# Optimization experiments

Hardware: AMD Instinct MI355X
Metric: run time of the kernel (lower is better)

## Reference

```python
import jax, jax.numpy as jnp
import numpy as np

B, S_IMG, S_TXT, P, D, HEADS, HD = 1, 2048, 512, 4, 3072, 24, 128


def rmsnorm(x, weight=None, eps=1e-6):
    var = jnp.mean(jnp.square(x), axis=-1, keepdims=True)
    y = x * jax.lax.rsqrt(var + eps)
    return y * weight if weight is not None else y


def apply_rope(x, cos, sin):
    # x: [B,H,S,Dh]; cos/sin: [S,Dh]; interleaved real/imag rotation (diffusers use_real_unbind_dim=-1)
    xr = x.reshape(*x.shape[:-1], -1, 2)
    rot = jnp.stack([-xr[..., 1], xr[..., 0]], axis=-1).reshape(x.shape)
    return x * cos[None, None] + rot * sin[None, None]


def sdpa(q, k, v):
    scores = jnp.einsum('bhqd,bhkd->bhqk', q, k) / jnp.sqrt(jnp.asarray(q.shape[-1], q.dtype))
    return jnp.einsum('bhqk,bhkd->bhqd', jax.nn.softmax(scores, axis=-1), v)


def heads_split(x):
    # [B,S,D] -> [B,H,S,Dh]
    return x.reshape(x.shape[0], x.shape[1], HEADS, HD).transpose(0, 2, 1, 3)


def heads_merge(x):
    # [B,H,S,Dh] -> [B,S,D]
    return x.transpose(0, 2, 1, 3).reshape(x.shape[0], x.shape[2], HEADS * HD)


def setup_inputs() -> dict:
    key = jax.random.key(0)
    ks = jax.random.split(key, 32)
    init = lambda k, shape: (jax.random.normal(k, shape, dtype=jnp.float32) * 0.02)
    inp = {
        'hidden_states': jax.random.normal(ks[0], (B, S_IMG, D), dtype=jnp.float32),
        'encoder_hidden_states': jax.random.normal(ks[1], (B, S_TXT, D), dtype=jnp.float32),
        'ip_encoder_hidden_states': jax.random.normal(ks[2], (B, P, D), dtype=jnp.float32),
        'layer_scale': jax.random.uniform(ks[3], (B,), dtype=jnp.float32),
        'Wq': init(ks[4], (D, D)), 'bq': jnp.zeros((D,), jnp.float32),
        'Wk': init(ks[5], (D, D)), 'bk': jnp.zeros((D,), jnp.float32),
        'Wv': init(ks[6], (D, D)), 'bv': jnp.zeros((D,), jnp.float32),
        'norm_q_w': jnp.ones((HD,), jnp.float32),
        'norm_k_w': jnp.ones((HD,), jnp.float32),
        'Waq': init(ks[7], (D, D)), 'baq': jnp.zeros((D,), jnp.float32),
        'Wak': init(ks[8], (D, D)), 'bak': jnp.zeros((D,), jnp.float32),
        'Wav': init(ks[9], (D, D)), 'bav': jnp.zeros((D,), jnp.float32),
        'norm_aq_w': jnp.ones((HD,), jnp.float32),
        'norm_ak_w': jnp.ones((HD,), jnp.float32),
        'Wk_ip': init(ks[10], (D, D)),
        'Wv_ip': init(ks[11], (D, D)),
        'Wo': init(ks[12], (D, D)), 'bo': jnp.zeros((D,), jnp.float32),
        'Wao': init(ks[13], (D, D)), 'bao': jnp.zeros((D,), jnp.float32),
    }
    # rotary cos/sin over the joint (text+image) sequence, interleaved freqs per diffusers FLUX
    pos = jnp.arange(S_TXT + S_IMG, dtype=jnp.float32)
    inv_freq = 1.0 / (10000.0 ** (jnp.arange(0, HD, 2, dtype=jnp.float32) / HD))
    angles = pos[:, None] * inv_freq[None, :]            # [S, HD/2]
    angles = jnp.repeat(angles, 2, axis=-1)              # [S, HD]
    inp['cos'] = jnp.cos(angles)
    inp['sin'] = jnp.sin(angles)
    return inp


IP_SCALE = 1.0  # self.scale


def reference(hidden_states, encoder_hidden_states, ip_encoder_hidden_states, cos, sin,
              layer_scale, Wq, bq, Wk, bk, Wv, bv, norm_q_w, norm_k_w,
              Waq, baq, Wak, bak, Wav, bav, norm_aq_w, norm_ak_w,
              Wk_ip, Wv_ip, Wo, bo, Wao, bao):
    # image-stream projections
    q = heads_split(hidden_states @ Wq.T + bq)
    k = heads_split(hidden_states @ Wk.T + bk)
    v = heads_split(hidden_states @ Wv.T + bv)
    q = rmsnorm(q, norm_q_w, 1e-6)
    k = rmsnorm(k, norm_k_w, 1e-6)

    # IP-adapter cross-attention (queries = image tokens, kv = IP tokens)
    ip_k = rmsnorm(heads_split(ip_encoder_hidden_states @ Wk_ip.T), None, 1e-5)
    ip_v = heads_split(ip_encoder_hidden_states @ Wv_ip.T)
    ip_out = heads_merge(sdpa(q, ip_k, ip_v))            # [B, S_img, D]

    # text (encoder) stream projections, prepended to joint sequence
    eq = rmsnorm(heads_split(encoder_hidden_states @ Waq.T + baq), norm_aq_w, 1e-6)
    ek = rmsnorm(heads_split(encoder_hidden_states @ Wak.T + bak), norm_ak_w, 1e-6)
    ev = heads_split(encoder_hidden_states @ Wav.T + bav)
    q = jnp.concatenate([eq, q], axis=2)
    k = jnp.concatenate([ek, k], axis=2)
    v = jnp.concatenate([ev, v], axis=2)

    q = apply_rope(q, cos, sin)
    k = apply_rope(k, cos, sin)

    out = heads_merge(sdpa(q, k, v))                     # [B, S_txt+S_img, D]
    n_txt = encoder_hidden_states.shape[1]
    enc_out, img_out = out[:, :n_txt], out[:, n_txt:]

    ls = layer_scale.reshape(-1, 1, 1)
    img_out = img_out + IP_SCALE * ls * ip_out
    img_out = img_out @ Wo.T + bo
    enc_out = enc_out @ Wao.T + bao
    return (img_out, enc_out)
```

## Files before the change

### kernel.cpp

```cpp
#include <hip/hip_runtime.h>

typedef _Float16 half_t;
typedef _Float16 half2v __attribute__((ext_vector_type(2)));
typedef _Float16 half4v __attribute__((ext_vector_type(4)));
typedef _Float16 half8v __attribute__((ext_vector_type(8)));
typedef float    float4v __attribute__((ext_vector_type(4)));
typedef short    short8v __attribute__((ext_vector_type(8)));

#define S_IMG 2048
#define S_TXT 512
#define S_TOT 2560
#define NH    24
#define HD    128
#define DM    3072

__device__ __forceinline__ void gload16(const void* g, void* l) {
  __builtin_amdgcn_global_load_lds(
      (const __attribute__((address_space(1))) unsigned int*)g,
      (__attribute__((address_space(3))) unsigned int*)l, 16, 0, 0);
}

__global__ void cvt_act_kernel(const float* __restrict__ hs, const float* __restrict__ enc,
                               half_t* __restrict__ d) {
  const long NHS = (long)S_IMG * DM;
  const long TOT = NHS + (long)S_TXT * DM;
  long i = ((long)blockIdx.x * 256 + threadIdx.x) * 8;
  long stride = (long)gridDim.x * 256 * 8;
  for (; i < TOT; i += stride) {
    const float* s = i < NHS ? hs + i : enc + (i - NHS);
    float4v v0 = *(const float4v*)(s);
    float4v v1 = *(const float4v*)(s + 4);
    half8v h;
    h[0] = (half_t)v0[0]; h[1] = (half_t)v0[1]; h[2] = (half_t)v0[2]; h[3] = (half_t)v0[3];
    h[4] = (half_t)v1[0]; h[5] = (half_t)v1[1]; h[6] = (half_t)v1[2]; h[7] = (half_t)v1[3];
    *(half8v*)(d + i) = h;
  }
}

__global__ void cvt3_kernel(const float* __restrict__ s0, const float* __restrict__ s1,
                            const float* __restrict__ s2,
                            half_t* __restrict__ d0, half_t* __restrict__ d1,
                            half_t* __restrict__ d2, int n) {
  const float* s = blockIdx.y == 0 ? s0 : (blockIdx.y == 1 ? s1 : s2);
  half_t* d = blockIdx.y == 0 ? d0 : (blockIdx.y == 1 ? d1 : d2);
  int i = (blockIdx.x * 256 + threadIdx.x) * 8;
  int stride = gridDim.x * 256 * 8;
  for (; i < n; i += stride) {
    float4v v0 = *(const float4v*)(s + i);
    float4v v1 = *(const float4v*)(s + i + 4);
    half8v h;
    h[0] = (half_t)v0[0]; h[1] = (half_t)v0[1]; h[2] = (half_t)v0[2]; h[3] = (half_t)v0[3];
    h[4] = (half_t)v1[0]; h[5] = (half_t)v1[1]; h[6] = (half_t)v1[2]; h[7] = (half_t)v1[3];
    *(half8v*)(d + i) = h;
  }
}

template <typename OUT>
__device__ __forceinline__ void gemm_tile(half_t* As, half_t* Bs,
                                          const half_t* __restrict__ A,
                                          const half_t* __restrict__ Bt,
                                          const float* __restrict__ bias,
                                          OUT* __restrict__ C, int bm, int bn) {
  const int K = DM, N = DM;
  const int tid = threadIdx.x, wid = tid >> 6, l = tid & 63;
  const int wm = (wid >> 1) * 64, wn = (wid & 1) * 64;
  const int l15 = l & 15, l4 = l >> 4;
  float4v acc[4][4] = {};

  const int scol = ((l & 3) ^ ((l >> 3) & 3)) * 8;
  const half_t* ga = A + (long)(bm + wid * 32 + (l >> 2)) * K + scol;
  const half_t* gb = Bt + (long)(bn + wid * 32 + (l >> 2)) * K + scol;
  const long rowstep = 16l * K;

#define GSTAGE(T, SEL)                                                        \
  {                                                                           \
    char* a_d = (char*)As + (SEL) * 8192 + wid * 2048;                        \
    char* b_d = (char*)Bs + (SEL) * 8192 + wid * 2048;                        \
    int k0 = (T) * 32;                                                        \
    gload16(ga + k0, a_d);                                                    \
    gload16(ga + rowstep + k0, a_d + 1024);                                   \
    gload16(gb + k0, b_d);                                                    \
    gload16(gb + rowstep + k0, b_d + 1024);                                   \
  }

  GSTAGE(0, 0);
  GSTAGE(1, 1);

  const int NT = K / 32;
  const int cofs = (l4 * 16) ^ (((l15 >> 1) & 3) << 4);
  for (int t = 0; t < NT; t++) {
    int cur = t % 3;
    if (t + 1 < NT) asm volatile("s_waitcnt vmcnt(4)" ::: "memory");
    else            asm volatile("s_waitcnt vmcnt(0)" ::: "memory");
    __builtin_amdgcn_s_barrier();
    __builtin_amdgcn_sched_barrier(0);
    if (t + 2 < NT) GSTAGE(t + 2, (t + 2) % 3);
    __builtin_amdgcn_sched_barrier(0);
    const char* AsB = (const char*)As + cur * 8192;
    const char* BsB = (const char*)Bs + cur * 8192;
    half8v af[4], bf[4];
#pragma unroll
    for (int i = 0; i < 4; i++)
      af[i] = *(const half8v*)(AsB + (wm + i * 16 + l15) * 64 + cofs);
#pragma unroll
    for (int j = 0; j < 4; j++)
      bf[j] = *(const half8v*)(BsB + (wn + j * 16 + l15) * 64 + cofs);
    __builtin_amdgcn_s_setprio(1);
#pragma unroll
    for (int i = 0; i < 4; i++)
#pragma unroll
      for (int j = 0; j < 4; j++)
        acc[i][j] = __builtin_amdgcn_mfma_f32_16x16x32_f16(af[i], bf[j], acc[i][j], 0, 0, 0);
    __builtin_amdgcn_s_setprio(0);
  }
#undef GSTAGE
#pragma unroll
  for (int i = 0; i < 4; i++)
#pragma unroll
    for (int j = 0; j < 4; j++) {
      int row = bm + wm + i * 16 + l4 * 4;
      int col = bn + wn + j * 16 + l15;
      float bv = bias ? bias[col] : 0.0f;
#pragma unroll
      for (int r = 0; r < 4; r++) {
        float v = acc[i][j][r] + bv;
        C[(long)(row + r) * N + col] = (OUT)v;
      }
    }
}

template <int NROW>
__global__ __launch_bounds__(256) void gemm3_kernel(const half_t* __restrict__ A,
                                                    const half_t* __restrict__ W0,
                                                    const half_t* __restrict__ W1,
                                                    const half_t* __restrict__ W2,
                                                    const float* b0, const float* b1, const float* b2,
                                                    half_t* O0, half_t* O1, half_t* O2) {
  __shared__ half_t As[3 * 128 * 32];
  __shared__ half_t Bs[3 * 128 * 32];
  int b = blockIdx.x;
  int q = (72 * NROW) >> 3;
  int wg = (b & 7) * q + (b >> 3);
  int col = wg / NROW, row = wg % NROW;
  int sel = col / 24;
  const half_t* Bt = sel == 0 ? W0 : (sel == 1 ? W1 : W2);
  const float* bias = sel == 0 ? b0 : (sel == 1 ? b1 : b2);
  half_t* C = sel == 0 ? O0 : (sel == 1 ? O1 : O2);
  gemm_tile<half_t>(As, Bs, A, Bt, bias, C, row * 128, (col % 24) * 128);
}

__global__ __launch_bounds__(256) void gemm_out_kernel(const half_t* __restrict__ ocomb,
                                                       const half_t* __restrict__ Wo_h,
                                                       const half_t* __restrict__ Wao_h,
                                                       const float* bo, const float* bao,
                                                       float* out_img, float* out_enc) {
  __shared__ half_t As[3 * 128 * 32];
  __shared__ half_t Bs[3 * 128 * 32];
  int b = blockIdx.x;
  int wg = (b & 7) * 60 + (b >> 3);
  int col = wg / 20, r = wg % 20;
  bool enc = r >= 16;
  const half_t* A = enc ? ocomb : ocomb + (long)S_TXT * DM;
  int bm = (enc ? (r - 16) : r) * 128;
  gemm_tile<float>(As, Bs, A, enc ? Wao_h : Wo_h, enc ? bao : bo,
                   enc ? out_enc : out_img, bm, col * 128);
}

__global__ __launch_bounds__(256) void ip_proj_kernel(const float* __restrict__ x,
                                                      const float* __restrict__ Wk_ip,
                                                      const float* __restrict__ Wv_ip,
                                                      float* __restrict__ outk,
                                                      float* __restrict__ outv) {
  const float* W = blockIdx.y ? Wv_ip : Wk_ip;
  float* out = blockIdx.y ? outv : outk;
  int n = blockIdx.x * 4 + (threadIdx.x >> 6);
  int l = threadIdx.x & 63;
  const float* wr = W + (long)n * DM;
  float acc[4] = {0.f, 0.f, 0.f, 0.f};
  for (int k = l * 4; k < DM; k += 256) {
    float4v wv = *(const float4v*)(wr + k);
#pragma unroll
    for (int p = 0; p < 4; p++) {
      float4v xv = *(const float4v*)(x + p * DM + k);
      acc[p] += wv[0] * xv[0] + wv[1] * xv[1] + wv[2] * xv[2] + wv[3] * xv[3];
    }
  }
#pragma unroll
  for (int off = 32; off; off >>= 1)
#pragma unroll
    for (int p = 0; p < 4; p++) acc[p] += __shfl_xor(acc[p], off, 64);
  if (l == 0)
#pragma unroll
    for (int p = 0; p < 4; p++) out[p * DM + n] = acc[p];
}

__global__ void ip_norm_kernel(const float* __restrict__ kr, const float* __restrict__ vr,
                               half_t* __restrict__ kh, half_t* __restrict__ vh) {
  int t = blockIdx.x;
  int l = threadIdx.x;
  int d = l * 2;
  if (t < 96) {
    int base = (t / 24) * DM + (t % 24) * HD;
    float x0 = kr[base + d], x1 = kr[base + d + 1];
    float ss = x0 * x0 + x1 * x1;
#pragma unroll
    for (int off = 32; off; off >>= 1) ss += __shfl_xor(ss, off, 64);
    float r = rsqrtf(ss * (1.0f / HD) + 1e-5f);
    kh[base + d] = (half_t)(x0 * r);
    kh[base + d + 1] = (half_t)(x1 * r);
  } else {
    int t2 = t - 96;
    int base = (t2 / 24) * DM + (t2 % 24) * HD;
    vh[base + d] = (half_t)vr[base + d];
    vh[base + d + 1] = (half_t)vr[base + d + 1];
  }
}

__global__ __launch_bounds__(256) void prep_kernel(
    const half_t* __restrict__ qraw, const half_t* __restrict__ kraw,
    const half_t* __restrict__ eq, const half_t* __restrict__ ek,
    const float* __restrict__ nqw, const float* __restrict__ nkw,
    const float* __restrict__ naqw, const float* __restrict__ nakw,
    const float* __restrict__ cosb, const float* __restrict__ sinb,
    half_t* __restrict__ qcat, half_t* __restrict__ kcat, half_t* __restrict__ qnr) {
  int task = blockIdx.x * 4 + (threadIdx.x >> 6);
  int l = threadIdx.x & 63;
  int s = task / NH, h = task - (task / NH) * NH;
  int d = l * 2;
  const half_t *qs, *ks;
  const float *wq, *wk;
  if (s < S_TXT) {
    long base = (long)s * DM + h * HD;
    qs = eq + base; ks = ek + base;
    wq = naqw; wk = nakw;
  } else {
    long base = (long)(s - S_TXT) * DM + h * HD;
    qs = qraw + base; ks = kraw + base;
    wq = nqw; wk = nkw;
  }
  half2v qv = *(const half2v*)(qs + d);
  half2v kv = *(const half2v*)(ks + d);
  float q0 = (float)qv[0], q1 = (float)qv[1];
  float k0 = (float)kv[0], k1 = (float)kv[1];
  float ssq = q0 * q0 + q1 * q1;
  float ssk = k0 * k0 + k1 * k1;
#pragma unroll
  for (int off = 32; off; off >>= 1) {
    ssq += __shfl_xor(ssq, off, 64);
    ssk += __shfl_xor(ssk, off, 64);
  }
  float rq = rsqrtf(ssq * (1.0f / HD) + 1e-6f);
  float rk = rsqrtf(ssk * (1.0f / HD) + 1e-6f);
  float qn0 = q0 * rq * wq[d], qn1 = q1 * rq * wq[d + 1];
  float kn0 = k0 * rk * wk[d], kn1 = k1 * rk * wk[d + 1];
  if (s >= S_TXT) {
    half2v o; o[0] = (half_t)qn0; o[1] = (half_t)qn1;
    *(half2v*)(qnr + ((long)h * S_IMG + (s - S_TXT)) * HD + d) = o;
  }
  float c0 = cosb[s * HD + d], c1 = cosb[s * HD + d + 1];
  float s0 = sinb[s * HD + d], s1 = sinb[s * HD + d + 1];
  float qo0 = qn0 * c0 - qn1 * s0, qo1 = qn1 * c1 + qn0 * s1;
  float ko0 = kn0 * c0 - kn1 * s0, ko1 = kn1 * c1 + kn0 * s1;
  long ci = ((long)h * S_TOT + s) * HD + d;
  half2v oq; oq[0] = (half_t)qo0; oq[1] = (half_t)qo1;
  half2v ok; ok[0] = (half_t)ko0; ok[1] = (half_t)ko1;
  *(half2v*)(qcat + ci) = oq;
  *(half2v*)(kcat + ci) = ok;
}

__global__ __launch_bounds__(256) void vtrans_kernel(const half_t* __restrict__ ev,
                                                     const half_t* __restrict__ vraw,
                                                     half_t* __restrict__ vcatT) {
  __shared__ half_t T[64][136];
  int h = blockIdx.y, sb = blockIdx.x * 64;
  int t = threadIdx.x;
#pragma unroll
  for (int i = 0; i < 4; i++) {
    int c = t + i * 256;
    int row = c >> 4, col = (c & 15) * 8;
    int s = sb + row;
    const half_t* src = (s < S_TXT) ? ev + (long)s * DM + h * HD + col
                                    : vraw + (long)(s - S_TXT) * DM + h * HD + col;
    *(half8v*)&T[row][col] = *(const half8v*)src;
  }
  __syncthreads();
#pragma unroll
  for (int i = 0; i < 4; i++) {
    int c = t + i * 256;
    int d = c >> 3, sc = (c & 7) * 8;
    half8v v;
#pragma unroll
    for (int j = 0; j < 8; j++) v[j] = T[sc + j][d];
    *(half8v*)(vcatT + ((long)h * HD + d) * S_TOT + sb + sc) = v;
  }
}

__global__ __launch_bounds__(256) void ip_attn_kernel(const half_t* __restrict__ qnr,
                                                      const half_t* __restrict__ kh,
                                                      const half_t* __restrict__ vh,
                                                      half_t* __restrict__ ipout) {
  int tid = threadIdx.x;
  int task = blockIdx.x * 16 + (tid >> 4);
  int l16 = tid & 15;
  int h = task >> 11;
  int s = task & 2047;
  int d = l16 * 8;
  half8v qv = *(const half8v*)(qnr + ((long)h * S_IMG + s) * HD + d);
  float sc[4];
#pragma unroll
  for (int p = 0; p < 4; p++) {
    half8v kv = *(const half8v*)(kh + p * DM + h * HD + d);
    float a = 0.f;
#pragma unroll
    for (int j = 0; j < 8; j++) a += (float)qv[j] * (float)kv[j];
    sc[p] = a;
  }
#pragma unroll
  for (int off = 8; off; off >>= 1)
#pragma unroll
    for (int p = 0; p < 4; p++) sc[p] += __shfl_xor(sc[p], off, 16);
  float m = fmaxf(fmaxf(sc[0], sc[1]), fmaxf(sc[2], sc[3]));
  float e[4], sum = 0.f;
#pragma unroll
  for (int p = 0; p < 4; p++) { e[p] = __expf((sc[p] - m) * 0.088388347648318447f); sum += e[p]; }
  float inv = 1.0f / sum;
  float o[8] = {};
#pragma unroll
  for (int p = 0; p < 4; p++) {
    half8v vv = *(const half8v*)(vh + p * DM + h * HD + d);
#pragma unroll
    for (int j = 0; j < 8; j++) o[j] += e[p] * (float)vv[j];
  }
  half8v ov;
#pragma unroll
  for (int j = 0; j < 8; j++) ov[j] = (half_t)(o[j] * inv);
  *(half8v*)(ipout + (long)s * DM + h * HD + d) = ov;
}

__global__ __launch_bounds__(256, 2) void flash_kernel(const half_t* __restrict__ qcat,
                                                       const half_t* __restrict__ kcat,
                                                       const half_t* __restrict__ vcatT,
                                                       const half_t* __restrict__ ipout,
                                                       const float* __restrict__ lsp,
                                                       half_t* __restrict__ ocomb) {
  __shared__ half_t Ks[2 * 64 * 128];
  __shared__ half_t Vs[128 * 64];
  __shared__ half_t Pw[4][32 * 72];
  int b = blockIdx.x;
  int wg = (b & 7) * 60 + (b >> 3);
  const int h = wg / 20, qb = wg % 20;
  const int tid = threadIdx.x, wid = tid >> 6, l = tid & 63;
  const int l15 = l & 15, l4 = l >> 4;
  const float CEXP = 0.12754137969983614f;

  half8v qf[2][4];
#pragma unroll
  for (int t = 0; t < 2; t++) {
    int qrow = qb * 128 + wid * 32 + t * 16 + l15;
    const half_t* qp = qcat + ((long)h * S_TOT + qrow) * HD;
#pragma unroll
    for (int kk = 0; kk < 4; kk++) qf[t][kk] = *(const half8v*)(qp + kk * 32 + l4 * 8);
  }
  float4v o[2][8] = {};
  float lreg[2] = {0.f, 0.f};
  const float ls = lsp[0];

  const char* kb = (const char*)(kcat + (long)h * S_TOT * HD);
  const char* vb = (const char*)(vcatT + (long)h * HD * S_TOT);
  int kof[4];
  long vof[4];
#pragma unroll
  for (int c = 0; c < 4; c++) {
    int L = c * 4096 + tid * 16;
    kof[c] = L ^ (((L >> 8) & 7) << 4);
    int vrow = L >> 7;
    vof[c] = (long)vrow * (S_TOT * 2) + ((L & 127) ^ ((vrow & 7) << 4));
  }

#define STAGE_K(KT, SEL)                                                      \
  {                                                                           \
    char* kd = (char*)Ks + (SEL) * 16384 + wid * 1024;                        \
    _Pragma("unroll") for (int c = 0; c < 4; c++)                             \
      gload16(kb + (long)(KT) * 256 + kof[c], kd + c * 4096);                 \
  }
#define STAGE_V(KT)                                                           \
  {                                                                           \
    char* vd = (char*)Vs + wid * 1024;                                        \
    _Pragma("unroll") for (int c = 0; c < 4; c++)                             \
      gload16(vb + vof[c] + (KT) * 2, vd + c * 4096);                         \
  }

  STAGE_K(0, 0);

  const int NT = S_TOT / 64;
  int sel = 0;
  for (int it = 0; it < NT; it++) {
    asm volatile("s_waitcnt vmcnt(0)" ::: "memory");
    __builtin_amdgcn_s_barrier();
    __builtin_amdgcn_sched_barrier(0);
    STAGE_V(it * 64);
    if (it + 1 < NT) STAGE_K((it + 1) * 64, sel ^ 1);

    const char* KsB = (const char*)Ks + sel * 16384;

    float4v s0[4] = {}, s1[4] = {};
    __builtin_amdgcn_s_setprio(1);
#pragma unroll
    for (int nb = 0; nb < 4; nb++) {
      int krow = nb * 16 + l15;
      int rb = krow << 8;
      int sw = (krow & 7) << 4;
#pragma unroll
      for (int kk = 0; kk < 4; kk++) {
        half8v kf = *(const half8v*)(KsB + rb + ((kk * 64 + l4 * 16) ^ sw));
        s0[nb] = __builtin_amdgcn_mfma_f32_16x16x32_f16(kf, qf[0][kk], s0[nb], 0, 0, 0);
        s1[nb] = __builtin_amdgcn_mfma_f32_16x16x32_f16(kf, qf[1][kk], s1[nb], 0, 0, 0);
      }
    }
    __builtin_amdgcn_s_setprio(0);
#pragma unroll
    for (int t = 0; t < 2; t++) {
      float4v* st = t ? s1 : s0;
      float sum = 0.f;
#pragma unroll
      for (int nb = 0; nb < 4; nb++) {
        half4v ph;
#pragma unroll
        for (int r = 0; r < 4; r++) {
          float e = exp2f(st[nb][r] * CEXP - 2.0f);
          sum += e;
          ph[r] = (half_t)e;
        }
        *(half4v*)&Pw[wid][(t * 16 + l15) * 72 + nb * 16 + l4 * 4] = ph;
      }
      sum += __shfl_xor(sum, 16, 64);
      sum += __shfl_xor(sum, 32, 64);
      lreg[t] += sum;
    }
    if (it + 1 < NT) asm volatile("s_waitcnt vmcnt(16)" ::: "memory");
    else             asm volatile("s_waitcnt vmcnt(0)" ::: "memory");
    __builtin_amdgcn_s_barrier();
    __builtin_amdgcn_sched_barrier(0);
    half8v pa00 = *(const half8v*)&Pw[wid][l15 * 72 + l4 * 8];
    half8v pa01 = *(const half8v*)&Pw[wid][l15 * 72 + 32 + l4 * 8];
    half8v pa10 = *(const half8v*)&Pw[wid][(16 + l15) * 72 + l4 * 8];
    half8v pa11 = *(const half8v*)&Pw[wid][(16 + l15) * 72 + 32 + l4 * 8];
    __builtin_amdgcn_s_setprio(1);
#pragma unroll
    for (int cb = 0; cb < 8; cb++) {
      int row = cb * 16 + l15;
      int sw = (row & 7) << 4;
      half8v vf0 = *(const half8v*)((const char*)Vs + (row << 7) + ((l4 * 16) ^ sw));
      half8v vf1 = *(const half8v*)((const char*)Vs + (row << 7) + ((64 + l4 * 16) ^ sw));
      o[0][cb] = __builtin_amdgcn_mfma_f32_16x16x32_f16(pa00, vf0, o[0][cb], 0, 0, 0);
      o[0][cb] = __builtin_amdgcn_mfma_f32_16x16x32_f16(pa01, vf1, o[0][cb], 0, 0, 0);
      o[1][cb] = __builtin_amdgcn_mfma_f32_16x16x32_f16(pa10, vf0, o[1][cb], 0, 0, 0);
      o[1][cb] = __builtin_amdgcn_mfma_f32_16x16x32_f16(pa11, vf1, o[1][cb], 0, 0, 0);
    }
    __builtin_amdgcn_s_setprio(0);
    sel ^= 1;
  }
#undef STAGE_K
#undef STAGE_V
#pragma unroll
  for (int t = 0; t < 2; t++) {
    float invq = 1.0f / lreg[t];
#pragma unroll
    for (int r = 0; r < 4; r++) {
      float inv = __shfl(invq, l4 * 4 + r, 64);
      int s = qb * 128 + wid * 32 + t * 16 + l4 * 4 + r;
#pragma unroll
      for (int cb = 0; cb < 8; cb++) {
        int col = h * HD + cb * 16 + l15;
        float val = o[t][cb][r] * inv;
        if (s >= S_TXT) val += ls * (float)ipout[(long)(s - S_TXT) * DM + col];
        ocomb[(long)s * DM + col] = (half_t)val;
      }
    }
  }
}

extern "C" void kernel_launch(void* const* d_in, const int* in_sizes, int n_in,
                              void* d_out, int out_size, void* d_ws, size_t ws_size,
                              hipStream_t stream) {
  (void)in_sizes; (void)n_in; (void)out_size; (void)ws_size;
  const float* hs    = (const float*)d_in[0];
  const float* enc   = (const float*)d_in[1];
  const float* ipenc = (const float*)d_in[2];
  const float* lsc   = (const float*)d_in[3];
  const float* Wq  = (const float*)d_in[4];  const float* bq  = (const float*)d_in[5];
  const float* Wk  = (const float*)d_in[6];  const float* bk  = (const float*)d_in[7];
  const float* Wv  = (const float*)d_in[8];  const float* bv  = (const float*)d_in[9];
  const float* nqw = (const float*)d_in[10]; const float* nkw = (const float*)d_in[11];
  const float* Waq = (const float*)d_in[12]; const float* baq = (const float*)d_in[13];
  const float* Wak = (const float*)d_in[14]; const float* bak = (const float*)d_in[15];
  const float* Wav = (const float*)d_in[16]; const float* bav = (const float*)d_in[17];
  const float* naqw= (const float*)d_in[18]; const float* nakw= (const float*)d_in[19];
  const float* Wkip= (const float*)d_in[20]; const float* Wvip= (const float*)d_in[21];
  const float* Wo  = (const float*)d_in[22]; const float* bo  = (const float*)d_in[23];
  const float* Wao = (const float*)d_in[24]; const float* bao = (const float*)d_in[25];
  const float* cosb= (const float*)d_in[26]; const float* sinb= (const float*)d_in[27];

  const size_t WSZ = (size_t)DM * DM;
  const size_t HSZ = (size_t)S_IMG * DM;
  const size_t ESZ = (size_t)S_TXT * DM;
  const size_t CSZ = (size_t)NH * S_TOT * HD;

  half_t* base = (half_t*)d_ws;
  half_t* W3    = base;
  half_t* hs_h  = W3 + 3 * WSZ;
  half_t* enc_h = hs_h + HSZ;
  half_t* qkvr  = enc_h + ESZ;
  half_t* eqkv  = qkvr + 3 * HSZ;
  half_t* qcat  = eqkv + 3 * ESZ;
  half_t* kcat  = qcat + CSZ;
  half_t* vcatT = kcat + CSZ;

  half_t* q_raw = qkvr;
  half_t* k_raw = qkvr + HSZ;
  half_t* v_raw = qkvr + 2 * HSZ;
  half_t* eq_r  = eqkv;
  half_t* ek_r  = eqkv + ESZ;
  half_t* ev_r  = eqkv + 2 * ESZ;
  half_t* qnr   = hs_h;
  half_t* ipout = qkvr;
  half_t* ocomb = qkvr + HSZ;
  float*  ipk_raw = (float*)enc_h;
  float*  ipv_raw = ipk_raw + 4 * DM;
  half_t* ipk_h  = enc_h + 16 * DM;
  half_t* ipv_h  = ipk_h + 4 * DM;

  cvt_act_kernel<<<2048, 256, 0, stream>>>(hs, enc, hs_h);

  cvt3_kernel<<<dim3(1024, 3), 256, 0, stream>>>(Wq, Wk, Wv, W3, W3 + WSZ, W3 + 2 * WSZ, (int)WSZ);
  gemm3_kernel<16><<<1152, 256, 0, stream>>>(hs_h, W3, W3 + WSZ, W3 + 2 * WSZ,
                                             bq, bk, bv, q_raw, k_raw, v_raw);
  cvt3_kernel<<<dim3(1024, 3), 256, 0, stream>>>(Waq, Wak, Wav, W3, W3 + WSZ, W3 + 2 * WSZ, (int)WSZ);
  gemm3_kernel<4><<<288, 256, 0, stream>>>(enc_h, W3, W3 + WSZ, W3 + 2 * WSZ,
                                           baq, bak, bav, eq_r, ek_r, ev_r);
  ip_proj_kernel<<<dim3(768, 2), 256, 0, stream>>>(ipenc, Wkip, Wvip, ipk_raw, ipv_raw);
  ip_norm_kernel<<<192, 64, 0, stream>>>(ipk_raw, ipv_raw, ipk_h, ipv_h);

  prep_kernel<<<(S_TOT * NH) / 4, 256, 0, stream>>>(q_raw, k_raw, eq_r, ek_r,
                                                    nqw, nkw, naqw, nakw, cosb, sinb,
                                                    qcat, kcat, qnr);
  vtrans_kernel<<<dim3(S_TOT / 64, NH), 256, 0, stream>>>(ev_r, v_raw, vcatT);

  ip_attn_kernel<<<(NH * S_IMG) / 16, 256, 0, stream>>>(qnr, ipk_h, ipv_h, ipout);

  flash_kernel<<<480, 256, 0, stream>>>(qcat, kcat, vcatT, ipout, lsc, ocomb);

  float* out_img = (float*)d_out;
  float* out_enc = (float*)d_out + (size_t)S_IMG * DM;
  cvt3_kernel<<<dim3(1024, 2), 256, 0, stream>>>(Wo, Wao, Wao, W3, W3 + WSZ, W3 + 2 * WSZ, (int)WSZ);
  gemm_out_kernel<<<480, 256, 0, stream>>>(ocomb, W3, W3 + WSZ, bo, bao, out_img, out_enc);
}
```

Measured before the change: 565.1 us.

## Load V fragments directly to registers and drop mid-iteration barrier

The flash kernel stops staging V tiles through shared memory. Each lane now loads its V MFMA fragments straight from global memory into registers at the start of every iteration. This removes the V LDS buffer, the second vmcnt wait and the second block barrier per iteration. The per-row softmax sum shuffles are also deferred to after the loop instead of running every tile. The trade-off is higher register pressure (16 extra half8v per lane) and strided, less coalesced global loads of V rows, which rely on L2 hits.

Result: slower. 614.9 us (+8.8%).

```diff
diff --git a/kernel.cpp b/kernel.cpp
--- a/kernel.cpp
+++ b/kernel.cpp
@@ -344,7 +344,6 @@
                                                        const float* __restrict__ lsp,
                                                        half_t* __restrict__ ocomb) {
   __shared__ half_t Ks[2 * 64 * 128];
-  __shared__ half_t Vs[128 * 64];
   __shared__ half_t Pw[4][32 * 72];
   int b = blockIdx.x;
   int wg = (b & 7) * 60 + (b >> 3);
@@ -362,19 +361,16 @@
     for (int kk = 0; kk < 4; kk++) qf[t][kk] = *(const half8v*)(qp + kk * 32 + l4 * 8);
   }
   float4v o[2][8] = {};
-  float lreg[2] = {0.f, 0.f};
+  float lsum[2] = {0.f, 0.f};
   const float ls = lsp[0];
 
   const char* kb = (const char*)(kcat + (long)h * S_TOT * HD);
-  const char* vb = (const char*)(vcatT + (long)h * HD * S_TOT);
+  const half_t* vb = vcatT + (long)h * HD * S_TOT;
   int kof[4];
-  long vof[4];
 #pragma unroll
   for (int c = 0; c < 4; c++) {
     int L = c * 4096 + tid * 16;
     kof[c] = L ^ (((L >> 8) & 7) << 4);
-    int vrow = L >> 7;
-    vof[c] = (long)vrow * (S_TOT * 2) + ((L & 127) ^ ((vrow & 7) << 4));
   }
 
 #define STAGE_K(KT, SEL)                                                      \
@@ -382,12 +378,6 @@
     char* kd = (char*)Ks + (SEL) * 16384 + wid * 1024;                        \
     _Pragma("unroll") for (int c = 0; c < 4; c++)                             \
       gload16(kb + (long)(KT) * 256 + kof[c], kd + c * 4096);                 \
-  }
-#define STAGE_V(KT)                                                           \
-  {                                                                           \
-    char* vd = (char*)Vs + wid * 1024;                                        \
-    _Pragma("unroll") for (int c = 0; c < 4; c++)                             \
-      gload16(vb + vof[c] + (KT) * 2, vd + c * 4096);                         \
   }
 
   STAGE_K(0, 0);
@@ -398,8 +388,15 @@
     asm volatile("s_waitcnt vmcnt(0)" ::: "memory");
     __builtin_amdgcn_s_barrier();
     __builtin_amdgcn_sched_barrier(0);
-    STAGE_V(it * 64);
+    half8v vf[2][8];
+#pragma unroll
+    for (int kk2 = 0; kk2 < 2; kk2++)
+#pragma unroll
+      for (int cb = 0; cb < 8; cb++)
+        vf[kk2][cb] = *(const half8v*)(vb + (long)(cb * 16 + l15) * S_TOT +
+                                       it * 64 + kk2 * 32 + l4 * 8);
     if (it + 1 < NT) STAGE_K((it + 1) * 64, sel ^ 1);
+    __builtin_amdgcn_sched_barrier(0);
 
     const char* KsB = (const char*)Ks + sel * 16384;
 
@@ -433,14 +430,8 @@
         }
         *(half4v*)&Pw[wid][(t * 16 + l15) * 72 + nb * 16 + l4 * 4] = ph;
       }
-      sum += __shfl_xor(sum, 16, 64);
-      sum += __shfl_xor(sum, 32, 64);
-      lreg[t] += sum;
+      lsum[t] += sum;
     }
-    if (it + 1 < NT) asm volatile("s_waitcnt vmcnt(16)" ::: "memory");
-    else             asm volatile("s_waitcnt vmcnt(0)" ::: "memory");
-    __builtin_amdgcn_s_barrier();
-    __builtin_amdgcn_sched_barrier(0);
     half8v pa00 = *(const half8v*)&Pw[wid][l15 * 72 + l4 * 8];
     half8v pa01 = *(const half8v*)&Pw[wid][l15 * 72 + 32 + l4 * 8];
     half8v pa10 = *(const half8v*)&Pw[wid][(16 + l15) * 72 + l4 * 8];
@@ -448,20 +439,23 @@
     __builtin_amdgcn_s_setprio(1);
 #pragma unroll
     for (int cb = 0; cb < 8; cb++) {
-      int row = cb * 16 + l15;
-      int sw = (row & 7) << 4;
-      half8v vf0 = *(const half8v*)((const char*)Vs + (row << 7) + ((l4 * 16) ^ sw));
-      half8v vf1 = *(const half8v*)((const char*)Vs + (row << 7) + ((64 + l4 * 16) ^ sw));
-      o[0][cb] = __builtin_amdgcn_mfma_f32_16x16x32_f16(pa00, vf0, o[0][cb], 0, 0, 0);
-      o[0][cb] = __builtin_amdgcn_mfma_f32_16x16x32_f16(pa01, vf1, o[0][cb], 0, 0, 0);
-      o[1][cb] = __builtin_amdgcn_mfma_f32_16x16x32_f16(pa10, vf0, o[1][cb], 0, 0, 0);
-      o[1][cb] = __builtin_amdgcn_mfma_f32_16x16x32_f16(pa11, vf1, o[1][cb], 0, 0, 0);
+      o[0][cb] = __builtin_amdgcn_mfma_f32_16x16x32_f16(pa00, vf[0][cb], o[0][cb], 0, 0, 0);
+      o[0][cb] = __builtin_amdgcn_mfma_f32_16x16x32_f16(pa01, vf[1][cb], o[0][cb], 0, 0, 0);
+      o[1][cb] = __builtin_amdgcn_mfma_f32_16x16x32_f16(pa10, vf[0][cb], o[1][cb], 0, 0, 0);
+      o[1][cb] = __builtin_amdgcn_mfma_f32_16x16x32_f16(pa11, vf[1][cb], o[1][cb], 0, 0, 0);
     }
     __builtin_amdgcn_s_setprio(0);
     sel ^= 1;
   }
 #undef STAGE_K
-#undef STAGE_V
+  float lreg[2];
+#pragma unroll
+  for (int t = 0; t < 2; t++) {
+    float s = lsum[t];
+    s += __shfl_xor(s, 16, 64);
+    s += __shfl_xor(s, 32, 64);
+    lreg[t] = s;
+  }
 #pragma unroll
   for (int t = 0; t < 2; t++) {
     float invq = 1.0f / lreg[t];
```
